# Kernel tuning notes

Measured on AMD Instinct MI355X. Metric: run time of the kernel, lower is better.

## Reference

```python
import jax, jax.numpy as jnp
import numpy as np


def setup_inputs() -> dict:
    key = jax.random.key(0)
    k1, k2, k3, k4 = jax.random.split(key, 4)
    B, S, D, F = 16, 4096, 1024, 1024
    x = jax.random.normal(k1, (B, S, D), dtype=jnp.float32)
    # Keras 'normal' initializer ~ N(0, 0.05); scale similarly for realism
    W_key = jax.random.normal(k2, (D, F), dtype=jnp.float32) * 0.05
    W_query = jax.random.normal(k3, (D, F), dtype=jnp.float32) * 0.05
    W_value = jax.random.normal(k4, (D, F), dtype=jnp.float32) * 0.05
    return {"x": x, "W_key": W_key, "W_query": W_query, "W_value": W_value}


def reference(x, W_key, W_query, W_value):
    # x: [B,S,D]; W_*: [D,F]
    keys = jnp.tanh(jnp.einsum("bsd,df->bsf", x, W_key))
    query = jnp.tanh(jnp.einsum("bsd,df->bsf", x, W_query))
    value = jnp.tanh(jnp.einsum("bsd,df->bsf", x, W_value))
    # diag(Q K^T) == per-token dot product, computed directly in O(S*F)
    attn_scores = jnp.einsum("bsf,bsf->bs", query, keys)  # [B,S]
    attn_softmax = jax.nn.softmax(attn_scores, axis=-1)[..., None]  # [B,S,1]
    # value^T @ softmax -> [B,F,1]
    weighted_input = jnp.einsum("bsf,bso->bfo", value, attn_softmax)
    return weighted_input, attn_softmax
```

## Files before the change

### kernel.cpp

```cpp
#include <hip/hip_runtime.h>
#include <hip/hip_bf16.h>
#include <math.h>
#include <stdint.h>

typedef _Float16 f16;
typedef _Float16 half8 __attribute__((ext_vector_type(8)));
typedef float f32x4 __attribute__((ext_vector_type(4)));

#define B_ 16
#define S_ 4096
#define D_ 1024
#define F_ 1024
#define TOK (B_*S_)
#define TB 128
#define FB 128
#define NFB (F_/FB)
#define BK 32
#define NS 16
#define CS (S_/NS)

__device__ __forceinline__ void gload_lds16(const void* g, void* l) {
    __builtin_amdgcn_global_load_lds(
        (__attribute__((address_space(1))) const unsigned int*)(unsigned long long)(uintptr_t)g,
        (__attribute__((address_space(3))) unsigned int*)(unsigned int)(uintptr_t)l,
        16, 0, 0);
}

__device__ __forceinline__ void fma4(float4& a, float s, const float4& wv) {
    a.x += s * wv.x; a.y += s * wv.y; a.z += s * wv.z; a.w += s * wv.w;
}
__device__ __forceinline__ void wtanh4(float4& acc, float pw, const float4& a) {
    acc.x += pw * tanhf(a.x); acc.y += pw * tanhf(a.y);
    acc.z += pw * tanhf(a.z); acc.w += pw * tanhf(a.w);
}

__global__ void cvt_x(const float* __restrict__ x, f16* __restrict__ xh) {
    size_t i = ((size_t)blockIdx.x * 256 + threadIdx.x) * 8;
    float4 a = *(const float4*)(x + i);
    float4 b = *(const float4*)(x + i + 4);
    half8 h = {(f16)a.x,(f16)a.y,(f16)a.z,(f16)a.w,
               (f16)b.x,(f16)b.y,(f16)b.z,(f16)b.w};
    *(half8*)(xh + i) = h;
}

__global__ void cvt_w(const float* __restrict__ Wk, const float* __restrict__ Wq,
                      f16* __restrict__ wt) {
    __shared__ float tile[32][33];
    const float* W = (blockIdx.z == 0) ? Wk : Wq;
    f16* outp = wt + (size_t)blockIdx.z * D_ * F_;
    int x0 = blockIdx.x * 32, y0 = blockIdx.y * 32;
    int tx = threadIdx.x, ty = threadIdx.y;
#pragma unroll
    for (int i = 0; i < 4; i++)
        tile[ty + i*8][tx] = W[(size_t)(y0 + ty + i*8) * F_ + x0 + tx];
    __syncthreads();
#pragma unroll
    for (int i = 0; i < 4; i++)
        outp[(size_t)(x0 + ty + i*8) * D_ + y0 + tx] = (f16)tile[tx][ty + i*8];
}

__launch_bounds__(256, 2)
__global__ void score_gemm(const f16* __restrict__ xh, const f16* __restrict__ wt,
                           float* __restrict__ part) {
    __shared__ __align__(16) f16 Xs[TB][32];
    __shared__ __align__(16) f16 WsK[FB][32];
    __shared__ __align__(16) f16 WsQ[FB][32];
    __shared__ float sred[2][TB];

    const int tok0 = blockIdx.x * TB;
    const int f0   = blockIdx.y * FB;
    const int t    = threadIdx.x;
    const int lane = t & 63;
    const int w    = t >> 6;
    const int wr   = (w >> 1) * 64;
    const int wc   = (w & 1) * 64;

    const int c0 = t, c1 = t + 256;
    const int r0 = c0 >> 2, q0 = (c0 & 3) * 8;
    const int r1 = c1 >> 2, q1 = (c1 & 3) * 8;
    char* ldsX = (char*)Xs  + (size_t)(t - lane) * 16;
    char* ldsK = (char*)WsK + (size_t)(t - lane) * 16;
    char* ldsQ = (char*)WsQ + (size_t)(t - lane) * 16;

    const f16* wK = wt + (size_t)f0 * D_;
    const f16* wQ = wt + (size_t)D_ * F_ + (size_t)f0 * D_;

    f32x4 accQ[4][4] = {};
    f32x4 accK[4][4] = {};

    for (int k0 = 0; k0 < D_; k0 += BK) {
        __syncthreads();
        gload_lds16(xh + (size_t)(tok0 + r0) * D_ + k0 + q0, ldsX);
        gload_lds16(xh + (size_t)(tok0 + r1) * D_ + k0 + q1, ldsX + 4096);
        gload_lds16(wK + (size_t)r0 * D_ + k0 + q0, ldsK);
        gload_lds16(wK + (size_t)r1 * D_ + k0 + q1, ldsK + 4096);
        gload_lds16(wQ + (size_t)r0 * D_ + k0 + q0, ldsQ);
        gload_lds16(wQ + (size_t)r1 * D_ + k0 + q1, ldsQ + 4096);
        __syncthreads();

        half8 aF[4], bK[4], bQ[4];
#pragma unroll
        for (int m = 0; m < 4; ++m)
            aF[m] = *(const half8*)&Xs[wr + m * 16 + (lane & 15)][(lane >> 4) * 8];
#pragma unroll
        for (int n = 0; n < 4; ++n) {
            bK[n] = *(const half8*)&WsK[wc + n * 16 + (lane & 15)][(lane >> 4) * 8];
            bQ[n] = *(const half8*)&WsQ[wc + n * 16 + (lane & 15)][(lane >> 4) * 8];
        }
#pragma unroll
        for (int n = 0; n < 4; ++n)
#pragma unroll
            for (int m = 0; m < 4; ++m) {
                accK[m][n] = __builtin_amdgcn_mfma_f32_16x16x32_f16(aF[m], bK[n], accK[m][n], 0, 0, 0);
                accQ[m][n] = __builtin_amdgcn_mfma_f32_16x16x32_f16(aF[m], bQ[n], accQ[m][n], 0, 0, 0);
            }
    }

#pragma unroll
    for (int m = 0; m < 4; ++m) {
        float s[4] = {0.f, 0.f, 0.f, 0.f};
#pragma unroll
        for (int n = 0; n < 4; ++n)
#pragma unroll
            for (int j = 0; j < 4; ++j)
                s[j] += tanhf(accQ[m][n][j]) * tanhf(accK[m][n][j]);
#pragma unroll
        for (int j = 0; j < 4; ++j) {
            s[j] += __shfl_xor(s[j], 1);
            s[j] += __shfl_xor(s[j], 2);
            s[j] += __shfl_xor(s[j], 4);
            s[j] += __shfl_xor(s[j], 8);
        }
        if ((lane & 15) == 0) {
            int g = lane >> 4;
#pragma unroll
            for (int j = 0; j < 4; ++j)
                sred[w & 1][wr + m * 16 + g * 4 + j] = s[j];
        }
    }
    __syncthreads();
    if (t < TB)
        part[(size_t)blockIdx.y * TOK + tok0 + t] = sred[0][t] + sred[1][t];
}

__global__ void softmax_k(const float* __restrict__ part, float* __restrict__ out) {
    __shared__ float sc[S_];
    __shared__ float red[256];
    const int b = blockIdx.x, t = threadIdx.x;
    float lmax = -1e30f;
    for (int i = t; i < S_; i += 256) {
        float s = 0.f;
#pragma unroll
        for (int fb = 0; fb < NFB; ++fb) s += part[(size_t)fb * TOK + b * S_ + i];
        sc[i] = s;
        lmax = fmaxf(lmax, s);
    }
    red[t] = lmax; __syncthreads();
    for (int o = 128; o > 0; o >>= 1) { if (t < o) red[t] = fmaxf(red[t], red[t + o]); __syncthreads(); }
    const float mx = red[0]; __syncthreads();
    float lsum = 0.f;
    for (int i = t; i < S_; i += 256) { float e = expf(sc[i] - mx); sc[i] = e; lsum += e; }
    red[t] = lsum; __syncthreads();
    for (int o = 128; o > 0; o >>= 1) { if (t < o) red[t] += red[t + o]; __syncthreads(); }
    const float inv = 1.0f / red[0];
    for (int i = t; i < S_; i += 256)
        out[(size_t)B_ * F_ + (size_t)b * S_ + i] = sc[i] * inv;
}

__launch_bounds__(256)
__global__ void value_k3(const float* __restrict__ x, const float* __restrict__ Wv,
                         const float* __restrict__ p_in, float* __restrict__ vpart) {
    __shared__ __align__(16) float xs[4][D_];
    __shared__ float ps[CS];
    __shared__ int   idxs[CS];
    __shared__ int   wsum[4];
    const int b = blockIdx.x, c = blockIdx.y;
    const int t = threadIdx.x, lane = t & 63, w = t >> 6;
    const int s0 = c * CS;

    float p = p_in[(size_t)b * S_ + s0 + t];
    bool flag = p > 1e-7f;
    unsigned long long mask = __ballot(flag);
    if (lane == 0) wsum[w] = __popcll(mask);
    __syncthreads();
    int base = 0;
#pragma unroll
    for (int i = 0; i < 4; ++i) if (i < w) base += wsum[i];
    const int cnt = wsum[0] + wsum[1] + wsum[2] + wsum[3];
    if (flag) {
        int pos = base + __popcll(mask & ((1ull << lane) - 1ull));
        idxs[pos] = s0 + t;
        ps[pos] = p;
    }
    __syncthreads();

    float4 acc = {0.f, 0.f, 0.f, 0.f};
    for (int g = 0; g < cnt; g += 4) {
        __syncthreads();
#pragma unroll
        for (int r = 0; r < 4; ++r) {
            float4 v = {0.f, 0.f, 0.f, 0.f};
            if (g + r < cnt)
                v = ((const float4*)(x + ((size_t)b * S_ + idxs[g + r]) * D_))[t];
            ((float4*)xs[r])[t] = v;
        }
        __syncthreads();
        float4 a0 = {0,0,0,0}, a1 = {0,0,0,0}, a2 = {0,0,0,0}, a3 = {0,0,0,0};
#pragma unroll 2
        for (int dq = 0; dq < D_ / 4; ++dq) {
            const float* wr = Wv + (size_t)dq * 4 * F_;
            float4 wv0 = ((const float4*)(wr        ))[t];
            float4 wv1 = ((const float4*)(wr + F_   ))[t];
            float4 wv2 = ((const float4*)(wr + 2*F_ ))[t];
            float4 wv3 = ((const float4*)(wr + 3*F_ ))[t];
            float4 x0 = ((const float4*)xs[0])[dq];
            float4 x1 = ((const float4*)xs[1])[dq];
            float4 x2 = ((const float4*)xs[2])[dq];
            float4 x3 = ((const float4*)xs[3])[dq];
            fma4(a0, x0.x, wv0); fma4(a0, x0.y, wv1); fma4(a0, x0.z, wv2); fma4(a0, x0.w, wv3);
            fma4(a1, x1.x, wv0); fma4(a1, x1.y, wv1); fma4(a1, x1.z, wv2); fma4(a1, x1.w, wv3);
            fma4(a2, x2.x, wv0); fma4(a2, x2.y, wv1); fma4(a2, x2.z, wv2); fma4(a2, x2.w, wv3);
            fma4(a3, x3.x, wv0); fma4(a3, x3.y, wv1); fma4(a3, x3.z, wv2); fma4(a3, x3.w, wv3);
        }
        int rem = cnt - g;
        if (rem > 0) wtanh4(acc, ps[g + 0], a0);
        if (rem > 1) wtanh4(acc, ps[g + 1], a1);
        if (rem > 2) wtanh4(acc, ps[g + 2], a2);
        if (rem > 3) wtanh4(acc, ps[g + 3], a3);
    }
    ((float4*)(vpart + ((size_t)c * B_ + b) * F_))[t] = acc;
}

__global__ void value_red(const float* __restrict__ vpart, float* __restrict__ out) {
    int i = blockIdx.x * 256 + threadIdx.x;
    float s = 0.f;
#pragma unroll
    for (int c = 0; c < NS; ++c) s += vpart[(size_t)c * B_ * F_ + i];
    out[i] = s;
}

extern "C" void kernel_launch(void* const* d_in, const int* in_sizes, int n_in,
                              void* d_out, int out_size, void* d_ws, size_t ws_size,
                              hipStream_t stream) {
    const float* x  = (const float*)d_in[0];
    const float* Wk = (const float*)d_in[1];
    const float* Wq = (const float*)d_in[2];
    const float* Wv = (const float*)d_in[3];
    float* out = (float*)d_out;
    char* ws = (char*)d_ws;

    f16*   xh   = (f16*)ws;
    f16*   wt   = (f16*)(ws + (size_t)TOK * D_ * 2);
    float* part = (float*)(ws + (size_t)TOK * D_ * 2 + 2 * (size_t)D_ * F_ * 2);

    cvt_x<<<TOK * D_ / 8 / 256, 256, 0, stream>>>(x, xh);
    cvt_w<<<dim3(32, 32, 2), dim3(32, 8), 0, stream>>>(Wk, Wq, wt);
    score_gemm<<<dim3(TOK / TB, NFB), 256, 0, stream>>>(xh, wt, part);
    softmax_k<<<B_, 256, 0, stream>>>(part, out);
    float* vpart = part;
    const float* p_in = out + (size_t)B_ * F_;
    value_k3<<<dim3(B_, NS), 256, 0, stream>>>(x, Wv, p_in, vpart);
    value_red<<<B_ * F_ / 256, 256, 0, stream>>>(vpart, out);
}
```

Baseline: 661.9 us.

## Double-buffer score GEMM LDS tiles with larger token and K blocks

Reworks the fused Q/K score GEMM to use 512-thread blocks covering 256 tokens and a K-step of 64. The X/K/Q shared-memory tiles are double-buffered so the next tile's global-to-LDS loads are issued before the current tile's MFMAs, with one barrier per iteration instead of two. The grid is also transposed so consecutive blocks share the same token tile across F-blocks, which may help L2 reuse of x. LDS use rises to about 130 KB per block, which limits how many blocks fit per CU, and the unpadded 128-byte rows may cause LDS bank conflicts.

```diff
diff --git a/kernel.cpp b/kernel.cpp
--- a/kernel.cpp
+++ b/kernel.cpp
@@ -12,10 +12,11 @@
 #define D_ 1024
 #define F_ 1024
 #define TOK (B_*S_)
-#define TB 128
+#define TB2 256
 #define FB 128
 #define NFB (F_/FB)
-#define BK 32
+#define BK2 64
+#define NT (D_/BK2)
 #define NS 16
 #define CS (S_/NS)
 
@@ -59,62 +60,78 @@
         outp[(size_t)(x0 + ty + i*8) * D_ + y0 + tx] = (f16)tile[tx][ty + i*8];
 }
 
-__launch_bounds__(256, 2)
+__launch_bounds__(512, 2)
 __global__ void score_gemm(const f16* __restrict__ xh, const f16* __restrict__ wt,
                            float* __restrict__ part) {
-    __shared__ __align__(16) f16 Xs[TB][32];
-    __shared__ __align__(16) f16 WsK[FB][32];
-    __shared__ __align__(16) f16 WsQ[FB][32];
-    __shared__ float sred[2][TB];
-
-    const int tok0 = blockIdx.x * TB;
-    const int f0   = blockIdx.y * FB;
+    __shared__ __align__(16) f16 Xs[2][TB2][BK2];
+    __shared__ __align__(16) f16 Ks[2][FB][BK2];
+    __shared__ __align__(16) f16 Qs[2][FB][BK2];
+    __shared__ float sred[2][TB2];
+
+    const int f0   = blockIdx.x * FB;
+    const int tok0 = blockIdx.y * TB2;
     const int t    = threadIdx.x;
     const int lane = t & 63;
     const int w    = t >> 6;
     const int wr   = (w >> 1) * 64;
     const int wc   = (w & 1) * 64;
 
-    const int c0 = t, c1 = t + 256;
-    const int r0 = c0 >> 2, q0 = (c0 & 3) * 8;
-    const int r1 = c1 >> 2, q1 = (c1 & 3) * 8;
-    char* ldsX = (char*)Xs  + (size_t)(t - lane) * 16;
-    char* ldsK = (char*)WsK + (size_t)(t - lane) * 16;
-    char* ldsQ = (char*)WsQ + (size_t)(t - lane) * 16;
-
     const f16* wK = wt + (size_t)f0 * D_;
     const f16* wQ = wt + (size_t)D_ * F_ + (size_t)f0 * D_;
 
+#define STAGE(bi, k0) do {                                                         \
+        char* xb = (char*)Xs[bi] + w * 1024;                                       \
+        char* kb = (char*)Ks[bi] + w * 1024;                                       \
+        char* qb = (char*)Qs[bi] + w * 1024;                                       \
+        _Pragma("unroll")                                                          \
+        for (int i_ = 0; i_ < 4; ++i_) {                                           \
+            int c_ = i_ * 512 + t;                                                 \
+            gload_lds16(xh + (size_t)(tok0 + (c_ >> 3)) * D_ + (k0) + (c_ & 7) * 8,\
+                        xb + i_ * 8192);                                           \
+        }                                                                          \
+        _Pragma("unroll")                                                          \
+        for (int i_ = 0; i_ < 2; ++i_) {                                           \
+            int c_ = i_ * 512 + t;                                                 \
+            gload_lds16(wK + (size_t)(c_ >> 3) * D_ + (k0) + (c_ & 7) * 8,         \
+                        kb + i_ * 8192);                                           \
+            gload_lds16(wQ + (size_t)(c_ >> 3) * D_ + (k0) + (c_ & 7) * 8,         \
+                        qb + i_ * 8192);                                           \
+        }                                                                          \
+    } while (0)
+
     f32x4 accQ[4][4] = {};
     f32x4 accK[4][4] = {};
 
-    for (int k0 = 0; k0 < D_; k0 += BK) {
+    STAGE(0, 0);
+    __syncthreads();
+    int cur = 0;
+
+    for (int kt = 0; kt < NT; ++kt) {
+        if (kt + 1 < NT) STAGE(cur ^ 1, (kt + 1) * BK2);
+
+#pragma unroll
+        for (int ks = 0; ks < 2; ++ks) {
+            half8 aF[4], bKf[4], bQf[4];
+#pragma unroll
+            for (int m = 0; m < 4; ++m)
+                aF[m] = *(const half8*)&Xs[cur][wr + m * 16 + (lane & 15)][ks * 32 + (lane >> 4) * 8];
+#pragma unroll
+            for (int n = 0; n < 4; ++n) {
+                bKf[n] = *(const half8*)&Ks[cur][wc + n * 16 + (lane & 15)][ks * 32 + (lane >> 4) * 8];
+                bQf[n] = *(const half8*)&Qs[cur][wc + n * 16 + (lane & 15)][ks * 32 + (lane >> 4) * 8];
+            }
+#pragma unroll
+            for (int n = 0; n < 4; ++n)
+#pragma unroll
+                for (int m = 0; m < 4; ++m) {
+                    accK[m][n] = __builtin_amdgcn_mfma_f32_16x16x32_f16(aF[m], bKf[n], accK[m][n], 0, 0, 0);
+                    accQ[m][n] = __builtin_amdgcn_mfma_f32_16x16x32_f16(aF[m], bQf[n], accQ[m][n], 0, 0, 0);
+                }
+        }
         __syncthreads();
-        gload_lds16(xh + (size_t)(tok0 + r0) * D_ + k0 + q0, ldsX);
-        gload_lds16(xh + (size_t)(tok0 + r1) * D_ + k0 + q1, ldsX + 4096);
-        gload_lds16(wK + (size_t)r0 * D_ + k0 + q0, ldsK);
-        gload_lds16(wK + (size_t)r1 * D_ + k0 + q1, ldsK + 4096);
-        gload_lds16(wQ + (size_t)r0 * D_ + k0 + q0, ldsQ);
-        gload_lds16(wQ + (size_t)r1 * D_ + k0 + q1, ldsQ + 4096);
-        __syncthreads();
-
-        half8 aF[4], bK[4], bQ[4];
-#pragma unroll
-        for (int m = 0; m < 4; ++m)
-            aF[m] = *(const half8*)&Xs[wr + m * 16 + (lane & 15)][(lane >> 4) * 8];
-#pragma unroll
-        for (int n = 0; n < 4; ++n) {
-            bK[n] = *(const half8*)&WsK[wc + n * 16 + (lane & 15)][(lane >> 4) * 8];
-            bQ[n] = *(const half8*)&WsQ[wc + n * 16 + (lane & 15)][(lane >> 4) * 8];
-        }
-#pragma unroll
-        for (int n = 0; n < 4; ++n)
-#pragma unroll
-            for (int m = 0; m < 4; ++m) {
-                accK[m][n] = __builtin_amdgcn_mfma_f32_16x16x32_f16(aF[m], bK[n], accK[m][n], 0, 0, 0);
-                accQ[m][n] = __builtin_amdgcn_mfma_f32_16x16x32_f16(aF[m], bQ[n], accQ[m][n], 0, 0, 0);
-            }
-    }
+        cur ^= 1;
+    }
+#undef STAGE
 
 #pragma unroll
     for (int m = 0; m < 4; ++m) {
@@ -139,8 +156,8 @@
         }
     }
     __syncthreads();
-    if (t < TB)
-        part[(size_t)blockIdx.y * TOK + tok0 + t] = sred[0][t] + sred[1][t];
+    if (t < TB2)
+        part[(size_t)blockIdx.x * TOK + tok0 + t] = sred[0][t] + sred[1][t];
 }
 
 __global__ void softmax_k(const float* __restrict__ part, float* __restrict__ out) {
@@ -255,7 +272,7 @@
 
     cvt_x<<<TOK * D_ / 8 / 256, 256, 0, stream>>>(x, xh);
     cvt_w<<<dim3(32, 32, 2), dim3(32, 8), 0, stream>>>(Wk, Wq, wt);
-    score_gemm<<<dim3(TOK / TB, NFB), 256, 0, stream>>>(xh, wt, part);
+    score_gemm<<<dim3(NFB, TOK / TB2), 512, 0, stream>>>(xh, wt, part);
     softmax_k<<<B_, 256, 0, stream>>>(part, out);
     float* vpart = part;
     const float* p_in = out + (size_t)B_ * F_;
```

Result: no change. 649.9 us (-1.8%).
